# Kernel tuning notes

Measured on AMD Instinct MI355X. Metric: run time of the kernel, lower is better.

## Reference

```python
import jax, jax.numpy as jnp
import numpy as np

N_NODES = 100000
N_EDGES = 1250000
D_FEAT = 64


def setup_inputs() -> dict:
    key = jax.random.key(0)
    k1, k2, k3 = jax.random.split(key, 3)
    inputs = jax.random.normal(k1, (N_NODES, D_FEAT), dtype=jnp.float32)
    src = jax.random.randint(k2, (N_EDGES,), 0, N_NODES, dtype=jnp.int32)
    dst = jax.random.randint(k3, (N_EDGES,), 0, N_NODES, dtype=jnp.int32)
    return {"inputs": inputs, "src": src, "dst": dst}


def reference(inputs, src, dst):
    # copy_src: message on each edge is the source node's feature -> gather
    msgs = inputs[src]  # [E, d]
    # gcn_reduce: max over mailbox (incoming messages) per destination node
    agg = jax.ops.segment_max(msgs, dst, num_segments=N_NODES)  # [N, d], -inf for empty
    # Nodes receiving no messages keep their original feature (DGL recv semantics)
    indeg = jax.ops.segment_sum(jnp.ones((src.shape[0],), dtype=jnp.int32), dst,
                                num_segments=N_NODES)  # [N]
    v_feature = jnp.where((indeg > 0)[:, None], agg, inputs)  # [N, d]
    return jnp.concatenate([inputs, v_feature], axis=1)  # [N, 2d]
```

## Files before the change

kernel.cpp:

```cpp
#include <hip/hip_runtime.h>
#include <math.h>

#define D_FEAT 64
#define SCAN_BLOCK 1024
#define N_RANGES 8


__global__ void zero_kernel(int* __restrict__ p, int n) {
    int i = blockIdx.x * blockDim.x + threadIdx.x;
    if (i < n) p[i] = 0;
}

__global__ void hist_part_kernel(const int* __restrict__ dst,
                                 int* __restrict__ counts,
                                 int n_edges, int nodes_per_range) {
    int r = blockIdx.x & (N_RANGES - 1);
    int c = blockIdx.x / N_RANGES;
    int nchunks = gridDim.x / N_RANGES;
    int lo = r * nodes_per_range;
    int hi = lo + nodes_per_range;
    int stride = nchunks * blockDim.x;
    for (int e = c * blockDim.x + threadIdx.x; e < n_edges; e += stride) {
        int d = dst[e];
        if (d >= lo && d < hi) atomicAdd(&counts[d], 1);
    }
}

__global__ void scanA_kernel(const int* __restrict__ counts,
                             int* __restrict__ offsets,
                             int* __restrict__ blocksums, int n) {
    __shared__ int smem[SCAN_BLOCK];
    int tid = threadIdx.x;
    int i = blockIdx.x * SCAN_BLOCK + tid;
    int v = (i < n) ? counts[i] : 0;
    smem[tid] = v;
    __syncthreads();
    for (int off = 1; off < SCAN_BLOCK; off <<= 1) {
        int t = (tid >= off) ? smem[tid - off] : 0;
        __syncthreads();
        smem[tid] += t;
        __syncthreads();
    }
    if (i < n) offsets[i] = smem[tid] - v;
    if (tid == SCAN_BLOCK - 1) blocksums[blockIdx.x] = smem[tid];
}

__global__ void scanB_kernel(int* __restrict__ blocksums, int nb) {
    __shared__ int smem[SCAN_BLOCK];
    int tid = threadIdx.x;
    int v = (tid < nb) ? blocksums[tid] : 0;
    smem[tid] = v;
    __syncthreads();
    for (int off = 1; off < SCAN_BLOCK; off <<= 1) {
        int t = (tid >= off) ? smem[tid - off] : 0;
        __syncthreads();
        smem[tid] += t;
        __syncthreads();
    }
    if (tid < nb) blocksums[tid] = smem[tid] - v;
}

__global__ void scanC_kernel(int* __restrict__ offsets, int* __restrict__ cursor,
                             const int* __restrict__ blocksums, int n, int n_edges) {
    int i = blockIdx.x * SCAN_BLOCK + threadIdx.x;
    if (i < n) {
        int o = offsets[i] + blocksums[blockIdx.x];
        offsets[i] = o;
        cursor[i] = o;
    }
    if (i == 0) offsets[n] = n_edges;
}

__global__ void scatter_part_kernel(const int* __restrict__ src,
                                    const int* __restrict__ dst,
                                    int* __restrict__ cursor,
                                    int* __restrict__ sorted_src,
                                    int n_edges, int nodes_per_range) {
    int r = blockIdx.x & (N_RANGES - 1);
    int c = blockIdx.x / N_RANGES;
    int nchunks = gridDim.x / N_RANGES;
    int lo = r * nodes_per_range;
    int hi = lo + nodes_per_range;
    int stride = nchunks * blockDim.x;
    for (int e = c * blockDim.x + threadIdx.x; e < n_edges; e += stride) {
        int d = dst[e];
        if (d >= lo && d < hi) {
            int pos = atomicAdd(&cursor[d], 1);
            sorted_src[pos] = src[e];
        }
    }
}

__global__ void pull_max_kernel(const float* __restrict__ inp,
                                const int* __restrict__ offsets,
                                const int* __restrict__ sorted_src,
                                float* __restrict__ out, int n_nodes) {
    int gtid = blockIdx.x * blockDim.x + threadIdx.x;
    int node = gtid >> 6;
    if (node >= n_nodes) return;
    int lane = threadIdx.x & 63;
    int g = lane >> 4;
    int l = lane & 15;

    int beg = offsets[node];
    int end = offsets[node + 1];

    const float4* inp4 = reinterpret_cast<const float4*>(inp);
    float4 own = inp4[(size_t)node * 16 + l];

    float4 m;
    m.x = -INFINITY; m.y = -INFINITY; m.z = -INFINITY; m.w = -INFINITY;
    for (int j = beg + g; j < end; j += 4) {
        int s = sorted_src[j];
        float4 v = inp4[(size_t)s * 16 + l];
        m.x = fmaxf(m.x, v.x);
        m.y = fmaxf(m.y, v.y);
        m.z = fmaxf(m.z, v.z);
        m.w = fmaxf(m.w, v.w);
    }
    m.x = fmaxf(m.x, __shfl_xor(m.x, 16, 64));
    m.y = fmaxf(m.y, __shfl_xor(m.y, 16, 64));
    m.z = fmaxf(m.z, __shfl_xor(m.z, 16, 64));
    m.w = fmaxf(m.w, __shfl_xor(m.w, 16, 64));
    m.x = fmaxf(m.x, __shfl_xor(m.x, 32, 64));
    m.y = fmaxf(m.y, __shfl_xor(m.y, 32, 64));
    m.z = fmaxf(m.z, __shfl_xor(m.z, 32, 64));
    m.w = fmaxf(m.w, __shfl_xor(m.w, 32, 64));

    if (beg == end) m = own;

    float4* out4 = reinterpret_cast<float4*>(out);
    if (lane < 16) {
        out4[(size_t)node * 32 + l] = own;
    } else if (lane < 32) {
        out4[(size_t)node * 32 + 16 + l] = m;
    }
}

extern "C" void kernel_launch(void* const* d_in, const int* in_sizes, int n_in,
                              void* d_out, int out_size, void* d_ws, size_t ws_size,
                              hipStream_t stream) {
    const float* inp = (const float*)d_in[0];
    const int* src = (const int*)d_in[1];
    const int* dst = (const int*)d_in[2];
    float* out = (float*)d_out;

    int n_nodes = in_sizes[0] / D_FEAT;
    int n_edges = in_sizes[1];

    int nScanBlocks = (n_nodes + SCAN_BLOCK - 1) / SCAN_BLOCK;
    int nodes_per_range = (n_nodes + N_RANGES - 1) / N_RANGES;

    int* ws = (int*)d_ws;
    int* counts_cursor = ws;
    int* offsets = ws + n_nodes;
    int* blocksums = ws + 2 * n_nodes + 1;
    int* sorted_src = ws + 2 * n_nodes + 1 + nScanBlocks;

    {
        int block = 256;
        int grid = (n_nodes + block - 1) / block;
        zero_kernel<<<grid, block, 0, stream>>>(counts_cursor, n_nodes);
    }
    hist_part_kernel<<<N_RANGES * 160, 256, 0, stream>>>(dst, counts_cursor,
                                                         n_edges, nodes_per_range);
    scanA_kernel<<<nScanBlocks, SCAN_BLOCK, 0, stream>>>(counts_cursor, offsets,
                                                         blocksums, n_nodes);
    scanB_kernel<<<1, SCAN_BLOCK, 0, stream>>>(blocksums, nScanBlocks);
    scanC_kernel<<<nScanBlocks, SCAN_BLOCK, 0, stream>>>(offsets, counts_cursor,
                                                         blocksums, n_nodes, n_edges);
    scatter_part_kernel<<<N_RANGES * 160, 256, 0, stream>>>(src, dst, counts_cursor,
                                                            sorted_src, n_edges,
                                                            nodes_per_range);
    {
        int total = n_nodes * 64;
        int block = 256;
        int grid = (total + block - 1) / block;
        pull_max_kernel<<<grid, block, 0, stream>>>(inp, offsets, sorted_src,
                                                    out, n_nodes);
    }
}
```

Before: 256.7 us.

## Use per-edge-group private counters for CSR build, warp-shuffle scan, unroll pull loop

Replaces the range-partitioned histogram, where every block scanned all edges and filtered by destination range, with 8 edge groups that each count into their own private counter array in a single pass. A fused scan turns the per-group counts into per-group starting positions, and scatter then places edges using offsets plus a per-group cursor. The scans switch to warp shuffles with no large shared array, and the pull loop is unrolled by two to keep more gathers in flight. In exchange it needs 8x node-sized workspace and adds a zeroing pass, and it falls back to the old path when the workspace is too small.

```diff
diff --git a/kernel.cpp b/kernel.cpp
--- a/kernel.cpp
+++ b/kernel.cpp
@@ -3,7 +3,8 @@
 
 #define D_FEAT 64
 #define SCAN_BLOCK 1024
-#define N_RANGES 8
+#define NG 8
+#define NR 8
 
 
 __global__ void zero_kernel(int* __restrict__ p, int n) {
@@ -11,12 +12,117 @@
     if (i < n) p[i] = 0;
 }
 
+__device__ __forceinline__ int block_scan_excl_1024(int v, int* smem16) {
+    int lane = threadIdx.x & 63;
+    int wid  = threadIdx.x >> 6;
+    int x = v;
+    #pragma unroll
+    for (int d = 1; d < 64; d <<= 1) {
+        int t = __shfl_up(x, d, 64);
+        if (lane >= d) x += t;
+    }
+    if (lane == 63) smem16[wid] = x;
+    __syncthreads();
+    if (wid == 0) {
+        int s = (lane < 16) ? smem16[lane] : 0;
+        #pragma unroll
+        for (int d = 1; d < 16; d <<= 1) {
+            int t = __shfl_up(s, d, 64);
+            if (lane >= d) s += t;
+        }
+        if (lane < 16) smem16[lane] = s;
+    }
+    __syncthreads();
+    int base = (wid > 0) ? smem16[wid - 1] : 0;
+    return base + x - v;
+}
+
+
+__global__ void count_group_kernel(const int* __restrict__ dst,
+                                   int* __restrict__ priv,
+                                   int n_nodes, int n_edges, int egroup) {
+    int g = blockIdx.x & (NG - 1);
+    int c = blockIdx.x >> 3;
+    int nchunks = gridDim.x >> 3;
+    int ebeg = g * egroup;
+    int eend = ebeg + egroup; if (eend > n_edges) eend = n_edges;
+    int* cnt = priv + (size_t)g * n_nodes;
+    int stride = nchunks * blockDim.x;
+    for (int e = ebeg + c * blockDim.x + threadIdx.x; e < eend; e += stride) {
+        atomicAdd(&cnt[dst[e]], 1);
+    }
+}
+
+__global__ void scanA_fused_kernel(int* __restrict__ priv,
+                                   int* __restrict__ offsets,
+                                   int* __restrict__ blocksums, int n_nodes) {
+    __shared__ int smem16[16];
+    int i = blockIdx.x * SCAN_BLOCK + threadIdx.x;
+    int total = 0;
+    if (i < n_nodes) {
+        int run = 0;
+        #pragma unroll
+        for (int g = 0; g < NG; ++g) {
+            size_t idx = (size_t)g * n_nodes + i;
+            int t = priv[idx];
+            priv[idx] = run;
+            run += t;
+        }
+        total = run;
+    }
+    int excl = block_scan_excl_1024(total, smem16);
+    if (i < n_nodes) offsets[i] = excl;
+    if (threadIdx.x == SCAN_BLOCK - 1) blocksums[blockIdx.x] = excl + total;
+}
+
+__global__ void scanB_kernel(int* __restrict__ blocksums, int nb) {
+    __shared__ int smem16[16];
+    int v = ((int)threadIdx.x < nb) ? blocksums[threadIdx.x] : 0;
+    int e = block_scan_excl_1024(v, smem16);
+    if ((int)threadIdx.x < nb) blocksums[threadIdx.x] = e;
+}
+
+__global__ void scanC_kernel(int* __restrict__ offsets,
+                             const int* __restrict__ blocksums,
+                             int n, int n_edges) {
+    int i = blockIdx.x * SCAN_BLOCK + threadIdx.x;
+    if (i < n) offsets[i] += blocksums[blockIdx.x];
+    if (i == 0) offsets[n] = n_edges;
+}
+
+__global__ void scatter_rg_kernel(const int* __restrict__ src,
+                                  const int* __restrict__ dst,
+                                  const int* __restrict__ offsets,
+                                  int* __restrict__ priv,
+                                  int* __restrict__ sorted_src,
+                                  int n_nodes, int n_edges, int egroup,
+                                  int nodes_per_range) {
+    int r = blockIdx.x & (NR - 1);
+    int g = (blockIdx.x >> 3) & (NG - 1);
+    int c = blockIdx.x >> 6;
+    int nchunks = gridDim.x >> 6;
+    int lo = r * nodes_per_range;
+    int hi = lo + nodes_per_range;
+    int ebeg = g * egroup;
+    int eend = ebeg + egroup; if (eend > n_edges) eend = n_edges;
+    int* cur = priv + (size_t)g * n_nodes;
+    int stride = nchunks * blockDim.x;
+    for (int e = ebeg + c * blockDim.x + threadIdx.x; e < eend; e += stride) {
+        int d = dst[e];
+        if (d >= lo && d < hi) {
+            int pos = offsets[d] + atomicAdd(&cur[d], 1);
+            sorted_src[pos] = src[e];
+        }
+    }
+}
+
+
 __global__ void hist_part_kernel(const int* __restrict__ dst,
                                  int* __restrict__ counts,
                                  int n_edges, int nodes_per_range) {
-    int r = blockIdx.x & (N_RANGES - 1);
-    int c = blockIdx.x / N_RANGES;
-    int nchunks = gridDim.x / N_RANGES;
+    int r = blockIdx.x & (NR - 1);
+    int c = blockIdx.x / NR;
+    int nchunks = gridDim.x / NR;
     int lo = r * nodes_per_range;
     int hi = lo + nodes_per_range;
     int stride = nchunks * blockDim.x;
@@ -26,42 +132,21 @@
     }
 }
 
-__global__ void scanA_kernel(const int* __restrict__ counts,
-                             int* __restrict__ offsets,
-                             int* __restrict__ blocksums, int n) {
-    __shared__ int smem[SCAN_BLOCK];
-    int tid = threadIdx.x;
-    int i = blockIdx.x * SCAN_BLOCK + tid;
+__global__ void scanA_plain_kernel(const int* __restrict__ counts,
+                                   int* __restrict__ offsets,
+                                   int* __restrict__ blocksums, int n) {
+    __shared__ int smem16[16];
+    int i = blockIdx.x * SCAN_BLOCK + threadIdx.x;
     int v = (i < n) ? counts[i] : 0;
-    smem[tid] = v;
-    __syncthreads();
-    for (int off = 1; off < SCAN_BLOCK; off <<= 1) {
-        int t = (tid >= off) ? smem[tid - off] : 0;
-        __syncthreads();
-        smem[tid] += t;
-        __syncthreads();
-    }
-    if (i < n) offsets[i] = smem[tid] - v;
-    if (tid == SCAN_BLOCK - 1) blocksums[blockIdx.x] = smem[tid];
-}
-
-__global__ void scanB_kernel(int* __restrict__ blocksums, int nb) {
-    __shared__ int smem[SCAN_BLOCK];
-    int tid = threadIdx.x;
-    int v = (tid < nb) ? blocksums[tid] : 0;
-    smem[tid] = v;
-    __syncthreads();
-    for (int off = 1; off < SCAN_BLOCK; off <<= 1) {
-        int t = (tid >= off) ? smem[tid - off] : 0;
-        __syncthreads();
-        smem[tid] += t;
-        __syncthreads();
-    }
-    if (tid < nb) blocksums[tid] = smem[tid] - v;
-}
-
-__global__ void scanC_kernel(int* __restrict__ offsets, int* __restrict__ cursor,
-                             const int* __restrict__ blocksums, int n, int n_edges) {
+    int e = block_scan_excl_1024(v, smem16);
+    if (i < n) offsets[i] = e;
+    if (threadIdx.x == SCAN_BLOCK - 1) blocksums[blockIdx.x] = e + v;
+}
+
+__global__ void scanC_plain_kernel(int* __restrict__ offsets,
+                                   int* __restrict__ cursor,
+                                   const int* __restrict__ blocksums,
+                                   int n, int n_edges) {
     int i = blockIdx.x * SCAN_BLOCK + threadIdx.x;
     if (i < n) {
         int o = offsets[i] + blocksums[blockIdx.x];
@@ -76,9 +161,9 @@
                                     int* __restrict__ cursor,
                                     int* __restrict__ sorted_src,
                                     int n_edges, int nodes_per_range) {
-    int r = blockIdx.x & (N_RANGES - 1);
-    int c = blockIdx.x / N_RANGES;
-    int nchunks = gridDim.x / N_RANGES;
+    int r = blockIdx.x & (NR - 1);
+    int c = blockIdx.x / NR;
+    int nchunks = gridDim.x / NR;
     int lo = r * nodes_per_range;
     int hi = lo + nodes_per_range;
     int stride = nchunks * blockDim.x;
@@ -90,6 +175,7 @@
         }
     }
 }
+
 
 __global__ void pull_max_kernel(const float* __restrict__ inp,
                                 const int* __restrict__ offsets,
@@ -110,7 +196,18 @@
 
     float4 m;
     m.x = -INFINITY; m.y = -INFINITY; m.z = -INFINITY; m.w = -INFINITY;
-    for (int j = beg + g; j < end; j += 4) {
+    int j = beg + g;
+    for (; j + 4 < end; j += 8) {
+        int s0 = sorted_src[j];
+        int s1 = sorted_src[j + 4];
+        float4 v0 = inp4[(size_t)s0 * 16 + l];
+        float4 v1 = inp4[(size_t)s1 * 16 + l];
+        m.x = fmaxf(m.x, fmaxf(v0.x, v1.x));
+        m.y = fmaxf(m.y, fmaxf(v0.y, v1.y));
+        m.z = fmaxf(m.z, fmaxf(v0.z, v1.z));
+        m.w = fmaxf(m.w, fmaxf(v0.w, v1.w));
+    }
+    if (j < end) {
         int s = sorted_src[j];
         float4 v = inp4[(size_t)s * 16 + l];
         m.x = fmaxf(m.x, v.x);
@@ -137,6 +234,7 @@
     }
 }
 
+
 extern "C" void kernel_launch(void* const* d_in, const int* in_sizes, int n_in,
                               void* d_out, int out_size, void* d_ws, size_t ws_size,
                               hipStream_t stream) {
@@ -149,34 +247,63 @@
     int n_edges = in_sizes[1];
 
     int nScanBlocks = (n_nodes + SCAN_BLOCK - 1) / SCAN_BLOCK;
-    int nodes_per_range = (n_nodes + N_RANGES - 1) / N_RANGES;
+    int nodes_per_range = (n_nodes + NR - 1) / NR;
+    int egroup = (n_edges + NG - 1) / NG;
 
     int* ws = (int*)d_ws;
-    int* counts_cursor = ws;
-    int* offsets = ws + n_nodes;
-    int* blocksums = ws + 2 * n_nodes + 1;
-    int* sorted_src = ws + 2 * n_nodes + 1 + nScanBlocks;
-
-    {
-        int block = 256;
-        int grid = (n_nodes + block - 1) / block;
-        zero_kernel<<<grid, block, 0, stream>>>(counts_cursor, n_nodes);
-    }
-    hist_part_kernel<<<N_RANGES * 160, 256, 0, stream>>>(dst, counts_cursor,
-                                                         n_edges, nodes_per_range);
-    scanA_kernel<<<nScanBlocks, SCAN_BLOCK, 0, stream>>>(counts_cursor, offsets,
-                                                         blocksums, n_nodes);
-    scanB_kernel<<<1, SCAN_BLOCK, 0, stream>>>(blocksums, nScanBlocks);
-    scanC_kernel<<<nScanBlocks, SCAN_BLOCK, 0, stream>>>(offsets, counts_cursor,
-                                                         blocksums, n_nodes, n_edges);
-    scatter_part_kernel<<<N_RANGES * 160, 256, 0, stream>>>(src, dst, counts_cursor,
-                                                            sorted_src, n_edges,
-                                                            nodes_per_range);
-    {
-        int total = n_nodes * 64;
-        int block = 256;
-        int grid = (total + block - 1) / block;
-        pull_max_kernel<<<grid, block, 0, stream>>>(inp, offsets, sorted_src,
-                                                    out, n_nodes);
-    }
-}
+    size_t need_main = ((size_t)NG * n_nodes + (size_t)(n_nodes + 1) +
+                        (size_t)nScanBlocks + (size_t)n_edges) * sizeof(int);
+
+    if (ws_size >= need_main) {
+        int* priv = ws;
+        int* offsets = ws + (size_t)NG * n_nodes;
+        int* blocksums = offsets + n_nodes + 1;
+        int* sorted_src = blocksums + nScanBlocks;
+
+        {
+            int total = NG * n_nodes;
+            zero_kernel<<<(total + 255) / 256, 256, 0, stream>>>(priv, total);
+        }
+        count_group_kernel<<<NG * 64, 256, 0, stream>>>(dst, priv, n_nodes,
+                                                        n_edges, egroup);
+        scanA_fused_kernel<<<nScanBlocks, SCAN_BLOCK, 0, stream>>>(priv, offsets,
+                                                                   blocksums, n_nodes);
+        scanB_kernel<<<1, SCAN_BLOCK, 0, stream>>>(blocksums, nScanBlocks);
+        scanC_kernel<<<nScanBlocks, SCAN_BLOCK, 0, stream>>>(offsets, blocksums,
+                                                             n_nodes, n_edges);
+        scatter_rg_kernel<<<NR * NG * 20, 256, 0, stream>>>(src, dst, offsets,
+                                                            priv, sorted_src,
+                                                            n_nodes, n_edges,
+                                                            egroup, nodes_per_range);
+        {
+            int total = n_nodes * 64;
+            pull_max_kernel<<<(total + 255) / 256, 256, 0, stream>>>(
+                inp, offsets, sorted_src, out, n_nodes);
+        }
+    } else {
+        int* counts_cursor = ws;
+        int* offsets = ws + n_nodes;
+        int* blocksums = offsets + n_nodes + 1;
+        int* sorted_src = blocksums + nScanBlocks;
+
+        zero_kernel<<<(n_nodes + 255) / 256, 256, 0, stream>>>(counts_cursor, n_nodes);
+        hist_part_kernel<<<NR * 160, 256, 0, stream>>>(dst, counts_cursor,
+                                                       n_edges, nodes_per_range);
+        scanA_plain_kernel<<<nScanBlocks, SCAN_BLOCK, 0, stream>>>(counts_cursor,
+                                                                   offsets, blocksums,
+                                                                   n_nodes);
+        scanB_kernel<<<1, SCAN_BLOCK, 0, stream>>>(blocksums, nScanBlocks);
+        scanC_plain_kernel<<<nScanBlocks, SCAN_BLOCK, 0, stream>>>(offsets,
+                                                                   counts_cursor,
+                                                                   blocksums,
+                                                                   n_nodes, n_edges);
+        scatter_part_kernel<<<NR * 160, 256, 0, stream>>>(src, dst, counts_cursor,
+                                                          sorted_src, n_edges,
+                                                          nodes_per_range);
+        {
+            int total = n_nodes * 64;
+            pull_max_kernel<<<(total + 255) / 256, 256, 0, stream>>>(
+                inp, offsets, sorted_src, out, n_nodes);
+        }
+    }
+}
```

After: 244.7 us. -4.7%, faster.
